# Optimization experiments

Measured on AMD Instinct MI355X. Metric: run time of the kernel, lower is better.

## Reference

```python
import jax, jax.numpy as jnp
import numpy as np

# Placement region / binning constants (match init_kwargs)
XL, YL, XH, YH = 0.0, 0.0, 512.0, 512.0
NBX, NBY = 512, 512
BSX = (XH - XL) / NBX  # 1.0
BSY = (YH - YL) / NBY  # 1.0
N = 5_000_000  # num_movable_nodes


def setup_inputs() -> dict:
    key = jax.random.key(0)
    k1, k2, k3, k4 = jax.random.split(key, 4)
    # pos = [x_0..x_{N-1}, y_0..y_{N-1}]; keep nodes inside the region
    pos = jax.random.uniform(k1, (2 * N,), jnp.float32) * (XH - 1.0)
    # LUT/FF instances are smaller than one bin -> at most a 2x2 bin window
    node_size_x = jax.random.uniform(k2, (N,), jnp.float32) * 0.9 + 0.05
    node_size_y = jax.random.uniform(k3, (N,), jnp.float32) * 0.9 + 0.05
    utilization_map = jax.random.uniform(k4, (NBX, NBY), jnp.float32) * 2.0
    flop_lut_indices = jnp.arange(N, dtype=jnp.int32)
    return {"pos": pos, "node_size_x": node_size_x, "node_size_y": node_size_y,
            "utilization_map": utilization_map, "flop_lut_indices": flop_lut_indices}


def _route_area(pos, sx, sy, umap):
    x = pos[:N]
    y = pos[N:2 * N]
    x_hi = x + sx
    y_hi = y + sy
    # lowest overlapped bin index per node
    bx0 = jnp.clip(jnp.floor((x - XL) / BSX).astype(jnp.int32), 0, NBX - 1)
    by0 = jnp.clip(jnp.floor((y - YL) / BSY).astype(jnp.int32), 0, NBY - 1)
    area = jnp.zeros((N,), jnp.float32)
    # node extent < bin size => at most a 2x2 window of bins overlaps each node
    for dx in range(2):
        bx = bx0 + dx
        bxl = XL + bx.astype(jnp.float32) * BSX
        ox = jnp.clip(jnp.minimum(x_hi, bxl + BSX) - jnp.maximum(x, bxl), 0.0, None)
        ox = jnp.where(bx < NBX, ox, 0.0)
        bxc = jnp.minimum(bx, NBX - 1)
        for dy in range(2):
            by = by0 + dy
            byl = YL + by.astype(jnp.float32) * BSY
            oy = jnp.clip(jnp.minimum(y_hi, byl + BSY) - jnp.maximum(y, byl), 0.0, None)
            oy = jnp.where(by < NBY, oy, 0.0)
            byc = jnp.minimum(by, NBY - 1)
            # irregular gather from the 2D utilization map
            area = area + ox * oy * umap[bxc, byc]
    return area


def reference(pos, node_size_x, node_size_y, utilization_map, flop_lut_indices):
    area = _route_area(pos, node_size_x, node_size_y, utilization_map)
    # only flop/lut instances receive a route area; others stay zero
    out = jnp.zeros((N,), jnp.float32).at[flop_lut_indices].set(area[flop_lut_indices])
    return out
```

## Files before the change

kernel.cpp:

```cpp
#include <hip/hip_runtime.h>

#define NBX 512
#define NBY 512

__global__ __launch_bounds__(256) void route_area_kernel(
    const float* __restrict__ pos,
    const float* __restrict__ nsx,
    const float* __restrict__ nsy,
    const float* __restrict__ umap,
    const int*   __restrict__ idx,
    float*       __restrict__ out,
    int n)
{
    int i = blockIdx.x * blockDim.x + threadIdx.x;
    if (i >= n) return;

    int j = idx[i];

    float x  = pos[j];
    float y  = pos[n + j];
    float sx = nsx[j];
    float sy = nsy[j];

    float x_hi = x + sx;
    float y_hi = y + sy;

    int bx0 = (int)floorf(x);
    bx0 = bx0 < 0 ? 0 : (bx0 > NBX - 1 ? NBX - 1 : bx0);
    int by0 = (int)floorf(y);
    by0 = by0 < 0 ? 0 : (by0 > NBY - 1 ? NBY - 1 : by0);

    float area = 0.0f;

    #pragma unroll
    for (int dx = 0; dx < 2; ++dx) {
        int bx = bx0 + dx;
        float bxl = (float)bx;
        float ox = fminf(x_hi, bxl + 1.0f) - fmaxf(x, bxl);
        ox = fmaxf(ox, 0.0f);
        if (bx >= NBX) ox = 0.0f;
        int bxc = bx < NBX - 1 ? bx : NBX - 1;

        #pragma unroll
        for (int dy = 0; dy < 2; ++dy) {
            int by = by0 + dy;
            float byl = (float)by;
            float oy = fminf(y_hi, byl + 1.0f) - fmaxf(y, byl);
            oy = fmaxf(oy, 0.0f);
            if (by >= NBY) oy = 0.0f;
            int byc = by < NBY - 1 ? by : NBY - 1;

            area = fmaf(ox * oy, umap[bxc * NBY + byc], area);
        }
    }

    out[j] = area;
}

extern "C" void kernel_launch(void* const* d_in, const int* in_sizes, int n_in,
                              void* d_out, int out_size, void* d_ws, size_t ws_size,
                              hipStream_t stream)
{
    const float* pos  = (const float*)d_in[0];
    const float* nsx  = (const float*)d_in[1];
    const float* nsy  = (const float*)d_in[2];
    const float* umap = (const float*)d_in[3];
    const int*   idx  = (const int*)d_in[4];
    float* out = (float*)d_out;

    int n = in_sizes[1];

    const int block = 256;
    const int grid  = (n + block - 1) / block;
    route_area_kernel<<<grid, block, 0, stream>>>(pos, nsx, nsy, umap, idx, out, n);
}
```

Measured before the change: 163.0 us.

## Pack 2x2 utilization neighbors into float4 table and vectorize identity-index fast path

Adds a pre-pass that builds a 512x512 float4 table holding each bin's 2x2 neighborhood of utilization values in workspace, so each node needs one 16-byte gather instead of four scattered loads. The main kernel now handles four nodes per thread with vectorized loads and stores when the index block is contiguous identity, and falls back to per-element scatter otherwise. This adds an extra 4 MB table write/read and a second launch, and keeps the old kernel as a fallback when workspace is too small.

```diff
diff --git a/kernel.cpp b/kernel.cpp
--- a/kernel.cpp
+++ b/kernel.cpp
@@ -3,7 +3,98 @@
 #define NBX 512
 #define NBY 512
 
-__global__ __launch_bounds__(256) void route_area_kernel(
+__global__ __launch_bounds__(256) void build_table_kernel(
+    const float* __restrict__ u, float4* __restrict__ W)
+{
+    int t = blockIdx.x * blockDim.x + threadIdx.x;
+    int bx = t >> 9;
+    int by = t & 511;
+    int bxp = bx + 1 < NBX ? bx + 1 : NBX - 1;
+    int byp = by + 1 < NBY ? by + 1 : NBY - 1;
+    float a = u[(bx  << 9) | by ];
+    float b = u[(bx  << 9) | byp];
+    float c = u[(bxp << 9) | by ];
+    float d = u[(bxp << 9) | byp];
+    W[t] = make_float4(a, b, c, d);
+}
+
+__device__ __forceinline__ float node_area(float x, float y, float sx, float sy,
+                                           const float4* __restrict__ W)
+{
+    float x_hi = x + sx;
+    float y_hi = y + sy;
+
+    int bx0 = (int)floorf(x);
+    bx0 = bx0 < 0 ? 0 : (bx0 > NBX - 1 ? NBX - 1 : bx0);
+    int by0 = (int)floorf(y);
+    by0 = by0 < 0 ? 0 : (by0 > NBY - 1 ? NBY - 1 : by0);
+
+    float bx0f = (float)bx0;
+    float by0f = (float)by0;
+
+    float ox0 = fmaxf(fminf(x_hi, bx0f + 1.0f) - fmaxf(x, bx0f), 0.0f);
+    float ox1 = fmaxf(fminf(x_hi, bx0f + 2.0f) - fmaxf(x, bx0f + 1.0f), 0.0f);
+    if (bx0 + 1 >= NBX) ox1 = 0.0f;
+
+    float oy0 = fmaxf(fminf(y_hi, by0f + 1.0f) - fmaxf(y, by0f), 0.0f);
+    float oy1 = fmaxf(fminf(y_hi, by0f + 2.0f) - fmaxf(y, by0f + 1.0f), 0.0f);
+    if (by0 + 1 >= NBY) oy1 = 0.0f;
+
+    float4 w = W[(bx0 << 9) | by0];
+
+    float area = ox0 * oy0 * w.x;
+    area = fmaf(ox0 * oy1, w.y, area);
+    area = fmaf(ox1 * oy0, w.z, area);
+    area = fmaf(ox1 * oy1, w.w, area);
+    return area;
+}
+
+__global__ __launch_bounds__(256) void route_area_v2_kernel(
+    const float*  __restrict__ pos,
+    const float*  __restrict__ nsx,
+    const float*  __restrict__ nsy,
+    const float4* __restrict__ W,
+    const int*    __restrict__ idx,
+    float*        __restrict__ out,
+    int n)
+{
+    int t = blockIdx.x * blockDim.x + threadIdx.x;
+    int base = t * 4;
+    if (base >= n) return;
+
+    if (base + 3 < n) {
+        int4 j4 = *(const int4*)(idx + base);
+        if (j4.x == base && j4.y == base + 1 && j4.z == base + 2 && j4.w == base + 3) {
+            float4 x4  = *(const float4*)(pos + base);
+            float4 y4  = *(const float4*)(pos + n + base);
+            float4 sx4 = *(const float4*)(nsx + base);
+            float4 sy4 = *(const float4*)(nsy + base);
+
+            float4 r;
+            r.x = node_area(x4.x, y4.x, sx4.x, sy4.x, W);
+            r.y = node_area(x4.y, y4.y, sx4.y, sy4.y, W);
+            r.z = node_area(x4.z, y4.z, sx4.z, sy4.z, W);
+            r.w = node_area(x4.w, y4.w, sx4.w, sy4.w, W);
+
+            *(float4*)(out + base) = r;
+            return;
+        }
+    }
+
+    #pragma unroll
+    for (int k = 0; k < 4; ++k) {
+        int i = base + k;
+        if (i >= n) break;
+        int j = idx[i];
+        float x  = pos[j];
+        float y  = pos[n + j];
+        float sx = nsx[j];
+        float sy = nsy[j];
+        out[j] = node_area(x, y, sx, sy, W);
+    }
+}
+
+__global__ __launch_bounds__(256) void route_area_v1_kernel(
     const float* __restrict__ pos,
     const float* __restrict__ nsx,
     const float* __restrict__ nsy,
@@ -16,12 +107,10 @@
     if (i >= n) return;
 
     int j = idx[i];
-
     float x  = pos[j];
     float y  = pos[n + j];
     float sx = nsx[j];
     float sy = nsy[j];
-
     float x_hi = x + sx;
     float y_hi = y + sy;
 
@@ -31,29 +120,23 @@
     by0 = by0 < 0 ? 0 : (by0 > NBY - 1 ? NBY - 1 : by0);
 
     float area = 0.0f;
-
     #pragma unroll
     for (int dx = 0; dx < 2; ++dx) {
         int bx = bx0 + dx;
         float bxl = (float)bx;
-        float ox = fminf(x_hi, bxl + 1.0f) - fmaxf(x, bxl);
-        ox = fmaxf(ox, 0.0f);
+        float ox = fmaxf(fminf(x_hi, bxl + 1.0f) - fmaxf(x, bxl), 0.0f);
         if (bx >= NBX) ox = 0.0f;
         int bxc = bx < NBX - 1 ? bx : NBX - 1;
-
         #pragma unroll
         for (int dy = 0; dy < 2; ++dy) {
             int by = by0 + dy;
             float byl = (float)by;
-            float oy = fminf(y_hi, byl + 1.0f) - fmaxf(y, byl);
-            oy = fmaxf(oy, 0.0f);
+            float oy = fmaxf(fminf(y_hi, byl + 1.0f) - fmaxf(y, byl), 0.0f);
             if (by >= NBY) oy = 0.0f;
             int byc = by < NBY - 1 ? by : NBY - 1;
-
             area = fmaf(ox * oy, umap[bxc * NBY + byc], area);
         }
     }
-
     out[j] = area;
 }
 
@@ -70,7 +153,17 @@
 
     int n = in_sizes[1];
 
-    const int block = 256;
-    const int grid  = (n + block - 1) / block;
-    route_area_kernel<<<grid, block, 0, stream>>>(pos, nsx, nsy, umap, idx, out, n);
+    const size_t table_bytes = (size_t)NBX * NBY * sizeof(float4);
+
+    if (ws_size >= table_bytes) {
+        float4* W = (float4*)d_ws;
+        build_table_kernel<<<(NBX * NBY) / 256, 256, 0, stream>>>(umap, W);
+
+        int threads = (n + 3) / 4;
+        int grid = (threads + 255) / 256;
+        route_area_v2_kernel<<<grid, 256, 0, stream>>>(pos, nsx, nsy, W, idx, out, n);
+    } else {
+        int grid = (n + 255) / 256;
+        route_area_v1_kernel<<<grid, 256, 0, stream>>>(pos, nsx, nsy, umap, idx, out, n);
+    }
 }
```

New measurement: 160.1 us. About the same (-1.8%).
